# Optimization experiments

Measured on AMD Instinct MI355X. Metric: run time of the kernel, lower is better.

The kernel has to match this reference:

```python
import jax, jax.numpy as jnp
import numpy as np

B, S, H, NH, DH, L, V, FF = 8, 512, 768, 12, 64, 12, 21128, 3072
PROMPT_LEN = 128
EPS = 1e-12  # BERT LayerNorm eps
NEG = -1e9


def _ln(x, g, b):
    m = jnp.mean(x, axis=-1, keepdims=True)
    xc = x - m
    v = jnp.mean(xc * xc, axis=-1, keepdims=True)
    return xc * jax.lax.rsqrt(v + EPS) * g + b


def setup_inputs() -> dict:
    key = jax.random.key(0)
    ks = jax.random.split(key, 16)
    def p(k, *shape):
        return (jax.random.normal(k, shape, jnp.float32) * 0.02)
    input_ids = jax.random.randint(ks[0], (B, S), 0, V)
    labels = jax.random.randint(ks[1], (B, S), 0, V)
    labels = labels.at[:, :PROMPT_LEN].set(-100)  # prefix = prompt, ignored in CE
    inp = dict(
        input_ids=input_ids,
        labels=labels,
        word_emb=p(ks[2], V, H),
        pos_emb=p(ks[3], S, H),
        type_emb=p(ks[4], 2, H),
        emb_ln_g=jnp.ones((H,), jnp.float32),
        emb_ln_b=jnp.zeros((H,), jnp.float32),
        Wq=p(ks[5], L, H, H), bq=jnp.zeros((L, H), jnp.float32),
        Wk=p(ks[6], L, H, H), bk=jnp.zeros((L, H), jnp.float32),
        Wv=p(ks[7], L, H, H), bv=jnp.zeros((L, H), jnp.float32),
        Wo=p(ks[8], L, H, H), bo=jnp.zeros((L, H), jnp.float32),
        ln1_g=jnp.ones((L, H), jnp.float32), ln1_b=jnp.zeros((L, H), jnp.float32),
        W1=p(ks[9], L, H, FF), bf1=jnp.zeros((L, FF), jnp.float32),
        W2=p(ks[10], L, FF, H), bf2=jnp.zeros((L, H), jnp.float32),
        ln2_g=jnp.ones((L, H), jnp.float32), ln2_b=jnp.zeros((L, H), jnp.float32),
        Wc=p(ks[11], H, V), bc=jnp.zeros((V,), jnp.float32),
    )
    return inp


def _forward(input_ids, labels, word_emb, pos_emb, type_emb, emb_ln_g, emb_ln_b,
             Wq, bq, Wk, bk, Wv, bv, Wo, bo, ln1_g, ln1_b,
             W1, bf1, W2, bf2, ln2_g, ln2_b, Wc, bc):
    # prefix-LM mask: prompt region fully bidirectional-visible, answer region causal
    prompt_len = jnp.sum(labels[0] == -100)
    i = jnp.arange(S)[:, None]
    j = jnp.arange(S)[None, :]
    mask = (j < prompt_len) | ((j >= prompt_len) & (j <= i))  # [S,S]
    bias = jnp.where(mask, 0.0, NEG).astype(jnp.float32)[None, None]  # [1,1,S,S]

    # embeddings (token_type_ids = 0)
    h = word_emb[input_ids] + pos_emb[None, :, :] + type_emb[0][None, None, :]
    h = _ln(h, emb_ln_g, emb_ln_b)
    scale = 1.0 / np.sqrt(DH).astype(np.float32)

    def layer(h, p):
        (wq, bq_, wk, bk_, wv, bv_, wo, bo_, g1, b1_, w1, bff1, w2, bff2, g2, b2_) = p
        q = (h @ wq + bq_).reshape(B, S, NH, DH).transpose(0, 2, 1, 3)
        k = (h @ wk + bk_).reshape(B, S, NH, DH).transpose(0, 2, 1, 3)
        v = (h @ wv + bv_).reshape(B, S, NH, DH).transpose(0, 2, 1, 3)
        scores = jnp.einsum('bhqd,bhkd->bhqk', q, k) * scale + bias
        attn = jax.nn.softmax(scores, axis=-1)
        ctx = jnp.einsum('bhqk,bhkd->bhqd', attn, v)
        ctx = ctx.transpose(0, 2, 1, 3).reshape(B, S, H)
        h = _ln(h + ctx @ wo + bo_, g1, b1_)
        ff = jax.nn.gelu(h @ w1 + bff1, approximate=False) @ w2 + bff2
        h = _ln(h + ff, g2, b2_)
        return h, None

    h, _ = jax.lax.scan(layer, h, (Wq, bq, Wk, bk, Wv, bv, Wo, bo, ln1_g, ln1_b,
                                   W1, bf1, W2, bf2, ln2_g, ln2_b))
    logits = h @ Wc + bc  # [B,S,V]

    # CrossEntropyLoss(ignore_index=-100), mean over valid tokens
    logp = jax.nn.log_softmax(logits, axis=-1)
    valid = labels != -100
    lab = jnp.where(valid, labels, 0)
    nll = -jnp.take_along_axis(logp, lab[..., None], axis=-1)[..., 0]
    loss = jnp.sum(nll * valid) / jnp.sum(valid).astype(jnp.float32)
    return loss


def reference(input_ids, labels, word_emb, pos_emb, type_emb, emb_ln_g, emb_ln_b,
              Wq, bq, Wk, bk, Wv, bv, Wo, bo, ln1_g, ln1_b,
              W1, bf1, W2, bf2, ln2_g, ln2_b, Wc, bc):
    return _forward(input_ids, labels, word_emb, pos_emb, type_emb, emb_ln_g, emb_ln_b,
                    Wq, bq, Wk, bk, Wv, bv, Wo, bo, ln1_g, ln1_b,
                    W1, bf1, W2, bf2, ln2_g, ln2_b, Wc, bc)
```

## Files before the change

kernel.cpp:

```cpp
#include <hip/hip_runtime.h>
#include <hip/hip_bf16.h>
#include <math.h>

#define BB 8
#define SS 512
#define HH 768
#define NHH 12
#define DHH 64
#define LL 12
#define VV 21128
#define VVP 21248
#define FFF 3072
#define TT (BB*SS)
#define PROMPT 128
#define LN_EPS 1e-12f
#define QKVN (3*HH)

typedef __attribute__((ext_vector_type(8))) short short8;
typedef __attribute__((ext_vector_type(4))) short short4v;
typedef __attribute__((ext_vector_type(4))) float floatx4;
typedef __attribute__((ext_vector_type(16))) float floatx16;

__device__ __forceinline__ float gelu_exact(float x) {
    return 0.5f * x * (1.0f + erff(x * 0.70710678118654752f));
}

__device__ __forceinline__ short f2bs(float x) {
    __hip_bfloat16 h = __float2bfloat16(x);
    return *reinterpret_cast<short*>(&h);
}

__device__ __forceinline__ int pack2(float a, float b) {
    const unsigned int lo = (unsigned short)f2bs(a);
    const unsigned int hi = (unsigned short)f2bs(b);
    return (int)(lo | (hi << 16));
}

union I4S8 { int i[4]; short8 s; };

__device__ __forceinline__ void load16_lds(const void* gptr, void* ldsptr) {
    __builtin_amdgcn_global_load_lds(
        (const __attribute__((address_space(1))) unsigned int*)(unsigned long long)(gptr),
        (__attribute__((address_space(3))) unsigned int*)(unsigned long long)(ldsptr),
        16, 0, 0);
}

__global__ __launch_bounds__(256) void gemm_mfma(
    const __hip_bfloat16* __restrict__ A,
    const __hip_bfloat16* __restrict__ Bt,
    const float* __restrict__ bias,
    float* __restrict__ Cf,
    __hip_bfloat16* __restrict__ Ch,
    int M, int N, int K, int act)
{
    __shared__ __hip_bfloat16 As[2][128 * 64];
    __shared__ __hip_bfloat16 Bs[2][128 * 64];

    const int tid  = threadIdx.x;
    const int wid  = tid >> 6;
    const int lane = tid & 63;
    const int row0 = blockIdx.y * 128;
    const int col0 = blockIdx.x * 128;

    const int wm = wid >> 1, wn = wid & 1;
    const int lr = lane >> 4, lc = lane & 15;

    const int nz   = gridDim.z;
    const int Kc   = K / nz;
    const int kbeg = blockIdx.z * Kc;
    if (nz > 1) Cf += (size_t)blockIdx.z * M * N;

    floatx4 acc[4][4] = {};

    const int sRow = tid >> 3;
    const int sC   = (tid & 7) ^ (sRow & 7);
    const __hip_bfloat16* aG[4];
    const __hip_bfloat16* bG[4];
    #pragma unroll
    for (int p = 0; p < 4; ++p) {
        aG[p] = A  + (size_t)(row0 + p * 32 + sRow) * K + kbeg + sC * 8;
        bG[p] = Bt + (size_t)(col0 + p * 32 + sRow) * K + kbeg + sC * 8;
    }

    const int nIter = Kc >> 6;

#define STAGE(buf, k0elem) do {                                      \
        char* aD = (char*)As + (buf) * 16384 + wid * 1024;           \
        char* bD = (char*)Bs + (buf) * 16384 + wid * 1024;           \
        _Pragma("unroll")                                            \
        for (int p = 0; p < 4; ++p) {                                \
            load16_lds(aG[p] + (k0elem), aD + p * 4096);             \
            load16_lds(bG[p] + (k0elem), bD + p * 4096);             \
        }                                                            \
    } while (0)

    STAGE(0, 0);
    __syncthreads();

    int cur = 0;
    for (int t = 0; t < nIter; ++t) {
        if (t + 1 < nIter) STAGE(cur ^ 1, (t + 1) << 6);

        const char* Ab = (const char*)As + cur * 16384;
        const char* Bb = (const char*)Bs + cur * 16384;

        __builtin_amdgcn_s_setprio(1);
        #pragma unroll
        for (int ks = 0; ks < 2; ++ks) {
            short8 af[4], bfr[4];
            #pragma unroll
            for (int mt = 0; mt < 4; ++mt) {
                const int row = wm * 64 + mt * 16 + lc;
                af[mt] = *(const short8*)(Ab + row * 128 +
                         ((((ks << 2) | lr) ^ (row & 7)) << 4));
            }
            #pragma unroll
            for (int nt = 0; nt < 4; ++nt) {
                const int row = wn * 64 + nt * 16 + lc;
                bfr[nt] = *(const short8*)(Bb + row * 128 +
                          ((((ks << 2) | lr) ^ (row & 7)) << 4));
            }
            #pragma unroll
            for (int mt = 0; mt < 4; ++mt)
                #pragma unroll
                for (int nt = 0; nt < 4; ++nt)
                    acc[mt][nt] = __builtin_amdgcn_mfma_f32_16x16x32_bf16(
                        af[mt], bfr[nt], acc[mt][nt], 0, 0, 0);
        }
        __builtin_amdgcn_s_setprio(0);

        __syncthreads();
        cur ^= 1;
    }
#undef STAGE

    #pragma unroll
    for (int mt = 0; mt < 4; ++mt) {
        #pragma unroll
        for (int nt = 0; nt < 4; ++nt) {
            const int n = col0 + wn * 64 + nt * 16 + lc;
            if (n < N) {
                #pragma unroll
                for (int r = 0; r < 4; ++r) {
                    const int m = row0 + wm * 64 + mt * 16 + lr * 4 + r;
                    float v = acc[mt][nt][r];
                    if (bias) v += bias[n];
                    if (act)  v = gelu_exact(v);
                    if (Cf) Cf[(size_t)m * N + n] = v;
                    if (Ch) Ch[(size_t)m * N + n] = __float2bfloat16(v);
                }
            }
        }
    }
}

__global__ void transpose_cvt(
    const float* __restrict__ W, __hip_bfloat16* __restrict__ out,
    int K, int N, long long in_lstride, long long out_lstride,
    int row_off, int out_ld)
{
    __shared__ float t[32][33];
    const int n0 = blockIdx.x * 32;
    const int k0 = blockIdx.y * 32;
    const int z  = blockIdx.z;
    const int tx = threadIdx.x, ty = threadIdx.y;

    const float* Wz = W + (size_t)z * in_lstride;
    __hip_bfloat16* Oz = out + (size_t)z * out_lstride;

    #pragma unroll
    for (int r = 0; r < 4; ++r) {
        const int k = k0 + ty + r * 8;
        const int n = n0 + tx;
        if (k < K && n < N) t[ty + r * 8][tx] = Wz[(size_t)k * N + n];
    }
    __syncthreads();
    #pragma unroll
    for (int r = 0; r < 4; ++r) {
        const int n = n0 + ty + r * 8;
        const int k = k0 + tx;
        if (n < N && k < K)
            Oz[(size_t)(row_off + n) * out_ld + k] = __float2bfloat16(t[tx][ty + r * 8]);
    }
}

__global__ void concat_bias(const float* __restrict__ bq, const float* __restrict__ bk,
                            const float* __restrict__ bv, float* __restrict__ bqkv)
{
    const int i = blockIdx.x * 256 + threadIdx.x;
    if (i >= LL * QKVN) return;
    const int l = i / QKVN, j = i % QKVN;
    float v;
    if (j < HH)            v = bq[l * HH + j];
    else if (j < 2 * HH)   v = bk[l * HH + j - HH];
    else                   v = bv[l * HH + j - 2 * HH];
    bqkv[i] = v;
}

__global__ __launch_bounds__(256) void embed_ln(
    const int* __restrict__ ids, const float* __restrict__ we,
    const float* __restrict__ pe, const float* __restrict__ te,
    const float* __restrict__ g, const float* __restrict__ b,
    __hip_bfloat16* __restrict__ h)
{
    const int t = blockIdx.x;
    const int s = t & (SS - 1);
    const int tid = threadIdx.x;
    __shared__ float x[HH];
    __shared__ float red[256];

    const int id = ids[t];
    for (int j = tid; j < HH; j += 256)
        x[j] = we[(size_t)id * HH + j] + pe[(size_t)s * HH + j] + te[j];
    __syncthreads();

    float sum = x[tid] + x[tid + 256] + x[tid + 512];
    red[tid] = sum; __syncthreads();
    for (int s2 = 128; s2 > 0; s2 >>= 1) { if (tid < s2) red[tid] += red[tid + s2]; __syncthreads(); }
    const float mean = red[0] * (1.0f / HH);
    __syncthreads();

    const float c0 = x[tid] - mean, c1 = x[tid + 256] - mean, c2 = x[tid + 512] - mean;
    red[tid] = c0 * c0 + c1 * c1 + c2 * c2; __syncthreads();
    for (int s2 = 128; s2 > 0; s2 >>= 1) { if (tid < s2) red[tid] += red[tid + s2]; __syncthreads(); }
    const float inv = rsqrtf(red[0] * (1.0f / HH) + LN_EPS);

    h[(size_t)t * HH + tid      ] = __float2bfloat16(c0 * inv * g[tid      ] + b[tid      ]);
    h[(size_t)t * HH + tid + 256] = __float2bfloat16(c1 * inv * g[tid + 256] + b[tid + 256]);
    h[(size_t)t * HH + tid + 512] = __float2bfloat16(c2 * inv * g[tid + 512] + b[tid + 512]);
}

__global__ __launch_bounds__(256) void add_ln(
    const __hip_bfloat16* __restrict__ resid, const float* __restrict__ y,
    int P, const float* __restrict__ bias,
    const float* __restrict__ g, const float* __restrict__ b,
    __hip_bfloat16* __restrict__ hout)
{
    const int t = blockIdx.x;
    const int tid = threadIdx.x;
    __shared__ float x[HH];
    __shared__ float red[256];

    for (int j = tid; j < HH; j += 256) {
        float s = __bfloat162float(resid[(size_t)t * HH + j]);
        if (bias) s += bias[j];
        for (int p = 0; p < P; ++p)
            s += y[(size_t)p * TT * HH + (size_t)t * HH + j];
        x[j] = s;
    }
    __syncthreads();

    float sum = x[tid] + x[tid + 256] + x[tid + 512];
    red[tid] = sum; __syncthreads();
    for (int s2 = 128; s2 > 0; s2 >>= 1) { if (tid < s2) red[tid] += red[tid + s2]; __syncthreads(); }
    const float mean = red[0] * (1.0f / HH);
    __syncthreads();

    const float c0 = x[tid] - mean, c1 = x[tid + 256] - mean, c2 = x[tid + 512] - mean;
    red[tid] = c0 * c0 + c1 * c1 + c2 * c2; __syncthreads();
    for (int s2 = 128; s2 > 0; s2 >>= 1) { if (tid < s2) red[tid] += red[tid + s2]; __syncthreads(); }
    const float inv = rsqrtf(red[0] * (1.0f / HH) + LN_EPS);

    hout[(size_t)t * HH + tid      ] = __float2bfloat16(c0 * inv * g[tid      ] + b[tid      ]);
    hout[(size_t)t * HH + tid + 256] = __float2bfloat16(c1 * inv * g[tid + 256] + b[tid + 256]);
    hout[(size_t)t * HH + tid + 512] = __float2bfloat16(c2 * inv * g[tid + 512] + b[tid + 512]);
}

__global__ __launch_bounds__(256) void attn_mfma(
    const __hip_bfloat16* __restrict__ qkv, __hip_bfloat16* __restrict__ ctx)
{
    const int qb  = blockIdx.x * 128;
    const int hh  = blockIdx.y;
    const int b   = blockIdx.z;
    const int tid = threadIdx.x;
    const int wid = tid >> 6;
    const int lane = tid & 63;
    const int lq = lane & 31;
    const int w  = lane >> 5;

    __shared__ __hip_bfloat16 Kb[64 * 64];
    __shared__ __hip_bfloat16 Vt[64 * 64];

    const int q0 = qb + wid * 32;
    const int i  = q0 + lq;

    short8 qf[4];
    {
        const __hip_bfloat16* qrow = qkv + (size_t)(b * SS + i) * QKVN + hh * DHH;
        #pragma unroll
        for (int kt = 0; kt < 4; ++kt)
            qf[kt] = *(const short8*)(qrow + kt * 16 + w * 8);
    }

    floatx16 acc_o[2] = {};
    float m_run = -1e30f, l_run = 0.f;

    const int kRow = tid >> 3;
    const int kC   = tid & 7;
    const int vd   = tid & 63;
    const int vk0  = (tid >> 6) << 4;

    const int kmax = (qb + 128 > PROMPT) ? (qb + 128) : PROMPT;

    for (int j0 = 0; j0 < kmax; j0 += 64) {
        #pragma unroll
        for (int x = 0; x < 2; ++x) {
            const int row = x * 32 + kRow;
            const __hip_bfloat16* src = qkv + (size_t)(b * SS + j0 + row) * QKVN
                                        + HH + hh * DHH + ((kC ^ (row & 7)) << 3);
            load16_lds(src, (char*)Kb + x * 4096 + wid * 1024 + (lane << 4));
        }
        {
            const short* vg = (const short*)(qkv + (size_t)(b * SS + j0 + vk0) * QKVN
                                             + 2 * HH + hh * DHH + vd);
            char* vrow = (char*)Vt + vd * 128;
            const int sw = (vd & 7) << 4;
            short8 v8a, v8b;
            #pragma unroll
            for (int x = 0; x < 8; ++x) v8a[x] = vg[(size_t)x * QKVN];
            #pragma unroll
            for (int x = 0; x < 8; ++x) v8b[x] = vg[(size_t)(x + 8) * QKVN];
            *(short8*)(vrow + ((vk0 << 1) ^ sw))        = v8a;
            *(short8*)(vrow + (((vk0 << 1) + 16) ^ sw)) = v8b;
        }
        __syncthreads();

        floatx16 s_acc[2];
        #pragma unroll
        for (int mt = 0; mt < 2; ++mt) {
            const char* krow = (const char*)Kb + (mt * 32 + lq) * 128;
            const int sw = (lq & 7) << 4;
            floatx16 acc = {};
            #pragma unroll
            for (int kt = 0; kt < 4; ++kt) {
                const short8 kf = *(const short8*)(krow + ((kt * 32 + w * 16) ^ sw));
                acc = __builtin_amdgcn_mfma_f32_32x32x16_bf16(kf, qf[kt], acc, 0, 0, 0);
            }
            s_acc[mt] = acc;
        }
        #pragma unroll
        for (int mt = 0; mt < 2; ++mt)
            #pragma unroll
            for (int r = 0; r < 16; ++r) s_acc[mt][r] *= 0.125f;

        const bool tfull = ((j0 + 63) < PROMPT) || ((j0 + 63) <= q0);
        if (!tfull) {
            #pragma unroll
            for (int mt = 0; mt < 2; ++mt)
                #pragma unroll
                for (int r = 0; r < 16; ++r) {
                    const int key = j0 + mt * 32 + (r & 3) + ((r >> 2) << 3) + (w << 2);
                    if (key >= PROMPT && key > i) s_acc[mt][r] = -1e30f;
                }
        }

        float tmax = -1e30f;
        #pragma unroll
        for (int mt = 0; mt < 2; ++mt)
            #pragma unroll
            for (int r = 0; r < 16; ++r) tmax = fmaxf(tmax, s_acc[mt][r]);
        tmax = fmaxf(tmax, __shfl_xor(tmax, 32, 64));
        const float mnew = fmaxf(m_run, tmax);
        const float corr = __expf(m_run - mnew);
        m_run = mnew;
        float psum = 0.f;
        #pragma unroll
        for (int mt = 0; mt < 2; ++mt)
            #pragma unroll
            for (int r = 0; r < 16; ++r) {
                const float p = __expf(s_acc[mt][r] - mnew);
                s_acc[mt][r] = p;
                psum += p;
            }
        l_run = l_run * corr + psum;
        #pragma unroll
        for (int r = 0; r < 16; ++r) { acc_o[0][r] *= corr; acc_o[1][r] *= corr; }

        short8 pbf[4];
        #pragma unroll
        for (int kt = 0; kt < 4; ++kt) {
            const int mt = kt >> 1;
            const int c0 = ((2 * kt) & 3) << 2;
            const int c1 = ((2 * kt + 1) & 3) << 2;
            const int w0 = pack2(s_acc[mt][c0 + 0], s_acc[mt][c0 + 1]);
            const int w1 = pack2(s_acc[mt][c0 + 2], s_acc[mt][c0 + 3]);
            const int w2 = pack2(s_acc[mt][c1 + 0], s_acc[mt][c1 + 1]);
            const int w3 = pack2(s_acc[mt][c1 + 2], s_acc[mt][c1 + 3]);
            const int t0 = __shfl_xor(w0, 32, 64);
            const int t1 = __shfl_xor(w1, 32, 64);
            const int t2 = __shfl_xor(w2, 32, 64);
            const int t3 = __shfl_xor(w3, 32, 64);
            I4S8 u;
            u.i[0] = w ? t2 : w0;
            u.i[1] = w ? t3 : w1;
            u.i[2] = w ? w2 : t0;
            u.i[3] = w ? w3 : t1;
            pbf[kt] = u.s;
        }

        #pragma unroll
        for (int mtd = 0; mtd < 2; ++mtd) {
            const char* vrow = (const char*)Vt + (mtd * 32 + lq) * 128;
            const int sw = (lq & 7) << 4;
            #pragma unroll
            for (int kt = 0; kt < 4; ++kt) {
                const short8 vf = *(const short8*)(vrow + ((kt * 32 + w * 16) ^ sw));
                acc_o[mtd] = __builtin_amdgcn_mfma_f32_32x32x16_bf16(vf, pbf[kt], acc_o[mtd], 0, 0, 0);
            }
        }
        __syncthreads();
    }

    const float lt  = l_run + __shfl_xor(l_run, 32, 64);
    const float inv = 1.0f / lt;
    __hip_bfloat16* crow = ctx + (size_t)(b * SS + i) * HH + hh * DHH;
    #pragma unroll
    for (int mtd = 0; mtd < 2; ++mtd)
        #pragma unroll
        for (int rq = 0; rq < 4; ++rq) {
            short4v o4;
            #pragma unroll
            for (int e = 0; e < 4; ++e)
                o4[e] = f2bs(acc_o[mtd][rq * 4 + e] * inv);
            *(short4v*)(crow + mtd * 32 + rq * 8 + w * 4) = o4;
        }
}

__global__ __launch_bounds__(256) void ce_kernel(
    const float* __restrict__ logits, const int* __restrict__ labels,
    int bidx, float* __restrict__ acc)
{
    const int r = blockIdx.x;
    const int t = bidx * SS + PROMPT + r;
    const float* row = logits + (size_t)r * VV;
    const int tid = threadIdx.x;
    __shared__ float redm[256];
    __shared__ float reds[256];

    float mx = -1e30f, se = 0.f;
    for (int c4 = tid; c4 < VV / 4; c4 += 256) {
        const float4 v = ((const float4*)row)[c4];
        const float lm = fmaxf(fmaxf(v.x, v.y), fmaxf(v.z, v.w));
        if (lm > mx) { se *= __expf(mx - lm); mx = lm; }
        se += __expf(v.x - mx) + __expf(v.y - mx) + __expf(v.z - mx) + __expf(v.w - mx);
    }
    redm[tid] = mx; reds[tid] = se; __syncthreads();
    for (int s2 = 128; s2 > 0; s2 >>= 1) {
        if (tid < s2) {
            const float m2 = redm[tid + s2], sv = reds[tid + s2];
            const float mN = fmaxf(redm[tid], m2);
            reds[tid] = reds[tid] * __expf(redm[tid] - mN) + sv * __expf(m2 - mN);
            redm[tid] = mN;
        }
        __syncthreads();
    }

    if (tid == 0) {
        const int lab = labels[t];
        if (lab >= 0) {
            const float nll = -(row[lab] - redm[0] - logf(reds[0]));
            atomicAdd(&acc[0], nll);
            atomicAdd(&acc[1], 1.0f);
        }
    }
}

__global__ void finalize_kernel(const float* __restrict__ acc, float* __restrict__ out)
{
    out[0] = (acc[1] > 0.f) ? acc[0] / acc[1] : 0.f;
}

extern "C" void kernel_launch(void* const* d_in, const int* in_sizes, int n_in,
                              void* d_out, int out_size, void* d_ws, size_t ws_size,
                              hipStream_t stream)
{
    const int*   input_ids = (const int*)  d_in[0];
    const int*   labels    = (const int*)  d_in[1];
    const float* word_emb  = (const float*)d_in[2];
    const float* pos_emb   = (const float*)d_in[3];
    const float* type_emb  = (const float*)d_in[4];
    const float* emb_ln_g  = (const float*)d_in[5];
    const float* emb_ln_b  = (const float*)d_in[6];
    const float* Wq = (const float*)d_in[7];   const float* bq = (const float*)d_in[8];
    const float* Wk = (const float*)d_in[9];   const float* bk = (const float*)d_in[10];
    const float* Wv = (const float*)d_in[11];  const float* bv = (const float*)d_in[12];
    const float* Wo = (const float*)d_in[13];  const float* bo = (const float*)d_in[14];
    const float* ln1_g = (const float*)d_in[15]; const float* ln1_b = (const float*)d_in[16];
    const float* W1 = (const float*)d_in[17];  const float* bf1 = (const float*)d_in[18];
    const float* W2 = (const float*)d_in[19];  const float* bf2 = (const float*)d_in[20];
    const float* ln2_g = (const float*)d_in[21]; const float* ln2_b = (const float*)d_in[22];
    const float* Wc = (const float*)d_in[23];  const float* bc = (const float*)d_in[24];

    float* fws  = (float*)d_ws;
    float* part = fws;
    float* lg   = fws;
    float* bqkv = fws + (size_t)TT * QKVN + (size_t)TT * HH;
    float* acc  = bqkv + (size_t)LL * QKVN;

    __hip_bfloat16* bws = (__hip_bfloat16*)(acc + 8);
    __hip_bfloat16* h    = bws;
    __hip_bfloat16* ctx  = h    + (size_t)TT * HH;
    __hip_bfloat16* ff1  = ctx  + (size_t)TT * HH;
    __hip_bfloat16* qkvb = ff1;
    __hip_bfloat16* qkvw = ff1  + (size_t)TT * FFF;
    __hip_bfloat16* wot  = qkvw + (size_t)LL * QKVN * HH;
    __hip_bfloat16* w1t  = wot  + (size_t)LL * HH * HH;
    __hip_bfloat16* w2t  = w1t  + (size_t)LL * FFF * HH;
    __hip_bfloat16* wct  = w2t  + (size_t)LL * HH * FFF;

    hipMemsetAsync(acc, 0, 2 * sizeof(float), stream);

    const dim3 tb(32, 8);
    transpose_cvt<<<dim3(24, 24, LL), tb, 0, stream>>>(Wq, qkvw, HH, HH,
        (long long)HH * HH, (long long)QKVN * HH, 0, HH);
    transpose_cvt<<<dim3(24, 24, LL), tb, 0, stream>>>(Wk, qkvw, HH, HH,
        (long long)HH * HH, (long long)QKVN * HH, HH, HH);
    transpose_cvt<<<dim3(24, 24, LL), tb, 0, stream>>>(Wv, qkvw, HH, HH,
        (long long)HH * HH, (long long)QKVN * HH, 2 * HH, HH);
    transpose_cvt<<<dim3(24, 24, LL), tb, 0, stream>>>(Wo, wot, HH, HH,
        (long long)HH * HH, (long long)HH * HH, 0, HH);
    transpose_cvt<<<dim3(96, 24, LL), tb, 0, stream>>>(W1, w1t, HH, FFF,
        (long long)HH * FFF, (long long)FFF * HH, 0, HH);
    transpose_cvt<<<dim3(24, 96, LL), tb, 0, stream>>>(W2, w2t, FFF, HH,
        (long long)FFF * HH, (long long)HH * FFF, 0, FFF);
    transpose_cvt<<<dim3(661, 24, 1), tb, 0, stream>>>(Wc, wct, HH, VV,
        0, 0, 0, HH);
    concat_bias<<<(LL * QKVN + 255) / 256, 256, 0, stream>>>(bq, bk, bv, bqkv);

    embed_ln<<<TT, 256, 0, stream>>>(input_ids, word_emb, pos_emb, type_emb,
                                     emb_ln_g, emb_ln_b, h);

    const dim3 gQKV(QKVN / 128, TT / 128, 1);
    const dim3 gWo (HH / 128,  TT / 128, 2);
    const dim3 gF  (FFF / 128, TT / 128, 1);
    const dim3 gFF2(HH / 128,  TT / 128, 3);
    const dim3 gAttn(SS / 128, NHH, BB);

    for (int l = 0; l < LL; ++l) {
        gemm_mfma<<<gQKV, 256, 0, stream>>>(h, qkvw + (size_t)l * QKVN * HH,
            bqkv + (size_t)l * QKVN, nullptr, qkvb, TT, QKVN, HH, 0);

        attn_mfma<<<gAttn, 256, 0, stream>>>(qkvb, ctx);

        gemm_mfma<<<gWo, 256, 0, stream>>>(ctx, wot + (size_t)l * HH * HH,
            nullptr, part, nullptr, TT, HH, HH, 0);
        add_ln<<<TT, 256, 0, stream>>>(h, part, 2, bo + (size_t)l * HH,
            ln1_g + (size_t)l * HH, ln1_b + (size_t)l * HH, h);

        gemm_mfma<<<gF, 256, 0, stream>>>(h, w1t + (size_t)l * FFF * HH,
            bf1 + (size_t)l * FFF, nullptr, ff1, TT, FFF, HH, 1);

        gemm_mfma<<<gFF2, 256, 0, stream>>>(ff1, w2t + (size_t)l * HH * FFF,
            nullptr, part, nullptr, TT, HH, FFF, 0);
        add_ln<<<TT, 256, 0, stream>>>(h, part, 3, bf2 + (size_t)l * HH,
            ln2_g + (size_t)l * HH, ln2_b + (size_t)l * HH, h);
    }

    const int Mchunk = SS - PROMPT;
    const dim3 gV(VVP / 128, Mchunk / 128, 1);
    for (int b = 0; b < BB; ++b) {
        const __hip_bfloat16* Arow = h + (size_t)(b * SS + PROMPT) * HH;
        gemm_mfma<<<gV, 256, 0, stream>>>(Arow, wct, bc, lg, nullptr, Mchunk, VV, HH, 0);
        ce_kernel<<<Mchunk, 256, 0, stream>>>(lg, labels, b, acc);
    }

    finalize_kernel<<<1, 1, 0, stream>>>(acc, (float*)d_out);
}
```

Before: 3.923 ms.

## Triple-buffer GEMM LDS pipeline and remap workgroups across XCDs

```diff
diff --git a/kernel.cpp b/kernel.cpp
--- a/kernel.cpp
+++ b/kernel.cpp
@@ -21,6 +21,8 @@
 typedef __attribute__((ext_vector_type(4))) float floatx4;
 typedef __attribute__((ext_vector_type(16))) float floatx16;
 
+#define GEMM_LDS_BYTES 98304
+
 __device__ __forceinline__ float gelu_exact(float x) {
     return 0.5f * x * (1.0f + erff(x * 0.70710678118654752f));
 }
@@ -53,14 +55,22 @@
     __hip_bfloat16* __restrict__ Ch,
     int M, int N, int K, int act)
 {
-    __shared__ __hip_bfloat16 As[2][128 * 64];
-    __shared__ __hip_bfloat16 Bs[2][128 * 64];
+    extern __shared__ char smem[];
 
     const int tid  = threadIdx.x;
     const int wid  = tid >> 6;
     const int lane = tid & 63;
-    const int row0 = blockIdx.y * 128;
-    const int col0 = blockIdx.x * 128;
+
+    const int gx  = gridDim.x;
+    const int nwg = gx * gridDim.y;
+    int flat = blockIdx.y * gx + blockIdx.x;
+    {
+        const int q = nwg >> 3, r = nwg & 7;
+        const int xcd = flat & 7, idx = flat >> 3;
+        flat = (xcd < r ? xcd * (q + 1) : r * (q + 1) + (xcd - r) * q) + idx;
+    }
+    const int row0 = (flat / gx) * 128;
+    const int col0 = (flat % gx) * 128;
 
     const int wm = wid >> 1, wn = wid & 1;
     const int lr = lane >> 4, lc = lane & 15;
@@ -84,25 +94,34 @@
 
     const int nIter = Kc >> 6;
 
-#define STAGE(buf, k0elem) do {                                      \
-        char* aD = (char*)As + (buf) * 16384 + wid * 1024;           \
-        char* bD = (char*)Bs + (buf) * 16384 + wid * 1024;           \
+#define STAGE(buf, kt) do {                                          \
+        char* aD = smem + (buf) * 32768 + wid * 1024;                \
+        char* bD = smem + (buf) * 32768 + 16384 + wid * 1024;        \
+        const int k0e = (kt) << 6;                                   \
         _Pragma("unroll")                                            \
         for (int p = 0; p < 4; ++p) {                                \
-            load16_lds(aG[p] + (k0elem), aD + p * 4096);             \
-            load16_lds(bG[p] + (k0elem), bD + p * 4096);             \
+            load16_lds(aG[p] + k0e, aD + p * 4096);                  \
+            load16_lds(bG[p] + k0e, bD + p * 4096);                  \
         }                                                            \
     } while (0)
 
     STAGE(0, 0);
-    __syncthreads();
-
-    int cur = 0;
+    if (nIter > 1) STAGE(1, 1);
+
+    int rs = 0;
     for (int t = 0; t < nIter; ++t) {
-        if (t + 1 < nIter) STAGE(cur ^ 1, (t + 1) << 6);
-
-        const char* Ab = (const char*)As + cur * 16384;
-        const char* Bb = (const char*)Bs + cur * 16384;
+        if (t + 1 < nIter) asm volatile("s_waitcnt vmcnt(8)" ::: "memory");
+        else               asm volatile("s_waitcnt vmcnt(0)" ::: "memory");
+        __builtin_amdgcn_s_barrier();
+        __builtin_amdgcn_sched_barrier(0);
+
+        if (t + 2 < nIter) {
+            int ss = rs + 2; if (ss >= 3) ss -= 3;
+            STAGE(ss, t + 2);
+        }
+
+        const char* Ab = smem + rs * 32768;
+        const char* Bb = Ab + 16384;
 
         __builtin_amdgcn_s_setprio(1);
         #pragma unroll
@@ -129,8 +148,7 @@
         }
         __builtin_amdgcn_s_setprio(0);
 
-        __syncthreads();
-        cur ^= 1;
+        if (++rs == 3) rs = 0;
     }
 #undef STAGE
 
@@ -491,6 +509,9 @@
     const float* ln2_g = (const float*)d_in[21]; const float* ln2_b = (const float*)d_in[22];
     const float* Wc = (const float*)d_in[23];  const float* bc = (const float*)d_in[24];
 
+    hipFuncSetAttribute(reinterpret_cast<const void*>(gemm_mfma),
+                        hipFuncAttributeMaxDynamicSharedMemorySize, GEMM_LDS_BYTES);
+
     float* fws  = (float*)d_ws;
     float* part = fws;
     float* lg   = fws;
@@ -537,20 +558,20 @@
     const dim3 gAttn(SS / 128, NHH, BB);
 
     for (int l = 0; l < LL; ++l) {
-        gemm_mfma<<<gQKV, 256, 0, stream>>>(h, qkvw + (size_t)l * QKVN * HH,
+        gemm_mfma<<<gQKV, 256, GEMM_LDS_BYTES, stream>>>(h, qkvw + (size_t)l * QKVN * HH,
             bqkv + (size_t)l * QKVN, nullptr, qkvb, TT, QKVN, HH, 0);
 
         attn_mfma<<<gAttn, 256, 0, stream>>>(qkvb, ctx);
 
-        gemm_mfma<<<gWo, 256, 0, stream>>>(ctx, wot + (size_t)l * HH * HH,
+        gemm_mfma<<<gWo, 256, GEMM_LDS_BYTES, stream>>>(ctx, wot + (size_t)l * HH * HH,
             nullptr, part, nullptr, TT, HH, HH, 0);
         add_ln<<<TT, 256, 0, stream>>>(h, part, 2, bo + (size_t)l * HH,
             ln1_g + (size_t)l * HH, ln1_b + (size_t)l * HH, h);
 
-        gemm_mfma<<<gF, 256, 0, stream>>>(h, w1t + (size_t)l * FFF * HH,
+        gemm_mfma<<<gF, 256, GEMM_LDS_BYTES, stream>>>(h, w1t + (size_t)l * FFF * HH,
             bf1 + (size_t)l * FFF, nullptr, ff1, TT, FFF, HH, 1);
 
-        gemm_mfma<<<gFF2, 256, 0, stream>>>(ff1, w2t + (size_t)l * HH * FFF,
+        gemm_mfma<<<gFF2, 256, GEMM_LDS_BYTES, stream>>>(ff1, w2t + (size_t)l * HH * FFF,
             nullptr, part, nullptr, TT, HH, FFF, 0);
         add_ln<<<TT, 256, 0, stream>>>(h, part, 3, bf2 + (size_t)l * HH,
             ln2_g + (size_t)l * HH, ln2_b + (size_t)l * HH, h);
@@ -560,7 +581,7 @@
     const dim3 gV(VVP / 128, Mchunk / 128, 1);
     for (int b = 0; b < BB; ++b) {
         const __hip_bfloat16* Arow = h + (size_t)(b * SS + PROMPT) * HH;
-        gemm_mfma<<<gV, 256, 0, stream>>>(Arow, wct, bc, lg, nullptr, Mchunk, VV, HH, 0);
+        gemm_mfma<<<gV, 256, GEMM_LDS_BYTES, stream>>>(Arow, wct, bc, lg, nullptr, Mchunk, VV, HH, 0);
         ce_kernel<<<Mchunk, 256, 0, stream>>>(lg, labels, b, acc);
     }
 
```

New measurement: 4.519 ms. +15.2%, slower.
